# Performance work log

Measured on AMD Instinct MI355X. Metric: run time of the kernel, lower is better.

## Reference

```python
import jax, jax.numpy as jnp
import numpy as np

HEAD_DIM = 128
NUM_HEADS = 16
NUM_KV_HEADS = 8
HIDDEN = 2048
SEQ = 4096
BATCH = 1
ROPE_THETA = 1e6
RMS_EPS = 1e-6


def rms_norm(x, w, eps=RMS_EPS):
    # normalize over the last (head_dim) axis
    var = jnp.mean(jnp.square(x), axis=-1, keepdims=True)
    return x * jax.lax.rsqrt(var + eps) * w


def apply_rope(x, positions):
    # x: [B, S, H, D], positions: [B, S]; rotate-half (GPT-NeoX style)
    d = x.shape[-1]
    inv_freq = 1.0 / (ROPE_THETA ** (jnp.arange(0, d, 2, dtype=jnp.float32) / d))  # [D/2]
    ang = positions.astype(jnp.float32)[..., None] * inv_freq  # [B, S, D/2]
    cos = jnp.cos(ang)[:, :, None, :]  # [B, S, 1, D/2]
    sin = jnp.sin(ang)[:, :, None, :]
    x1, x2 = x[..., : d // 2], x[..., d // 2 :]
    return jnp.concatenate([x1 * cos - x2 * sin, x2 * cos + x1 * sin], axis=-1)


def setup_inputs() -> dict:
    key = jax.random.key(0)
    ks = jax.random.split(key, 8)
    s = 0.02
    return {
        "positions": jnp.broadcast_to(jnp.arange(SEQ, dtype=jnp.int64 if jax.config.jax_enable_x64 else jnp.int32)[None, :], (BATCH, SEQ)),
        "hidden_states": jax.random.normal(ks[0], (BATCH, SEQ, HIDDEN), jnp.float32),
        "wq": jax.random.normal(ks[1], (NUM_HEADS * HEAD_DIM, HIDDEN), jnp.float32) * s,
        "bq": jnp.zeros((NUM_HEADS * HEAD_DIM,), jnp.float32),
        "wk": jax.random.normal(ks[2], (NUM_KV_HEADS * HEAD_DIM, HIDDEN), jnp.float32) * s,
        "bk": jnp.zeros((NUM_KV_HEADS * HEAD_DIM,), jnp.float32),
        "wv": jax.random.normal(ks[3], (NUM_KV_HEADS * HEAD_DIM, HIDDEN), jnp.float32) * s,
        "bv": jnp.zeros((NUM_KV_HEADS * HEAD_DIM,), jnp.float32),
        "wo": jax.random.normal(ks[4], (HIDDEN, NUM_HEADS * HEAD_DIM), jnp.float32) * s,
        "bo": jnp.zeros((HIDDEN,), jnp.float32),
        "q_norm_w": jnp.ones((HEAD_DIM,), jnp.float32),
        "k_norm_w": jnp.ones((HEAD_DIM,), jnp.float32),
    }


def reference(positions, hidden_states, wq, bq, wk, bk, wv, bv, wo, bo, q_norm_w, k_norm_w):
    B, S, _ = hidden_states.shape
    H, Hkv, D = NUM_HEADS, NUM_KV_HEADS, HEAD_DIM
    scaling = D ** -0.5

    q = (hidden_states @ wq.T + bq).reshape(B, S, H, D)
    k = (hidden_states @ wk.T + bk).reshape(B, S, Hkv, D)
    v = (hidden_states @ wv.T + bv).reshape(B, S, Hkv, D)

    q = apply_rope(rms_norm(q, q_norm_w), positions)
    k = apply_rope(rms_norm(k, k_norm_w), positions)

    # GQA: repeat_interleave kv heads to match query heads
    rep = H // Hkv
    k = jnp.repeat(k, rep, axis=2)  # [B, S, H, D]
    v = jnp.repeat(v, rep, axis=2)

    # scores: [B, H, S, S]
    scores = jnp.einsum("bqhd,bkhd->bhqk", q, k) * scaling
    causal = jnp.tril(jnp.ones((S, S), dtype=bool))
    scores = jnp.where(causal[None, None], scores, -jnp.inf)
    attn = jax.nn.softmax(scores, axis=-1)

    out = jnp.einsum("bhqk,bkhd->bqhd", attn, v).reshape(B, S, H * D)
    return out @ wo.T + bo
```

## Files before the change

kernel.cpp:

```cpp
#include <hip/hip_runtime.h>
#include <hip/hip_bf16.h>

#define SQ   4096
#define HIDN 2048
#define NH   16
#define NKV  8
#define HD   128
#define QD   2048
#define KD   1024
#define KVB  64

typedef __bf16 bf16x8 __attribute__((ext_vector_type(8)));
typedef float  f32x4  __attribute__((ext_vector_type(4)));

__device__ __forceinline__ float b2f(unsigned short u) {
    union { float f; unsigned int i; } v; v.i = ((unsigned int)u) << 16; return v.f;
}
__device__ __forceinline__ unsigned short f2b(float f) {
    union { float f; unsigned int i; } v; v.f = f;
    unsigned int i = v.i;
    return (unsigned short)((i + 0x7FFFu + ((i >> 16) & 1u)) >> 16);
}

__device__ __forceinline__ void gload_lds16(const void* g, void* l) {
    __builtin_amdgcn_global_load_lds(
        (const __attribute__((address_space(1))) unsigned int*)g,
        (__attribute__((address_space(3))) unsigned int*)l, 16, 0, 0);
}

#define MFMA16(a, b, c) __builtin_amdgcn_mfma_f32_16x16x32_bf16(a, b, c, 0, 0, 0)

#define DPP_ROR(x, n) __int_as_float(__builtin_amdgcn_update_dpp(            \
    __float_as_int(x), __float_as_int(x), 0x120 + (n), 0xF, 0xF, false))

__device__ __forceinline__ float rowmax16(float x) {
    x = fmaxf(x, DPP_ROR(x, 1));
    x = fmaxf(x, DPP_ROR(x, 2));
    x = fmaxf(x, DPP_ROR(x, 4));
    x = fmaxf(x, DPP_ROR(x, 8));
    return x;
}
__device__ __forceinline__ float rowsum16(float x) {
    x += DPP_ROR(x, 1);
    x += DPP_ROR(x, 2);
    x += DPP_ROR(x, 4);
    x += DPP_ROR(x, 8);
    return x;
}

__global__ __launch_bounds__(256) void cvt_all(const float* __restrict__ h,
                                               const float* __restrict__ wq,
                                               const float* __restrict__ wk,
                                               const float* __restrict__ wv,
                                               const float* __restrict__ wo,
                                               unsigned short* __restrict__ oh,
                                               unsigned short* __restrict__ owq,
                                               unsigned short* __restrict__ owk,
                                               unsigned short* __restrict__ owv,
                                               unsigned short* __restrict__ owo) {
    int i = blockIdx.x * 256 + threadIdx.x;
    const float* src; unsigned short* dst; int off;
    if (i < 2097152)      { src = h;  dst = oh;  off = i; }
    else if (i < 3145728) { src = wq; dst = owq; off = i - 2097152; }
    else if (i < 3670016) { src = wk; dst = owk; off = i - 3145728; }
    else if (i < 4194304) { src = wv; dst = owv; off = i - 3670016; }
    else                  { src = wo; dst = owo; off = i - 4194304; }
    float4 v = ((const float4*)src)[off];
    ushort4 u;
    u.x = f2b(v.x); u.y = f2b(v.y); u.z = f2b(v.z); u.w = f2b(v.w);
    ((ushort4*)dst)[off] = u;
}

__global__ __launch_bounds__(256) void rope_table(const int* __restrict__ pos,
                                                  float* __restrict__ cosT,
                                                  float* __restrict__ sinT) {
    int i = blockIdx.x * 256 + threadIdx.x;
    int s = i >> 6, j = i & 63;
    double invf = exp(-(double)j * (log(1.0e6) / 64.0));
    float a = (float)((double)pos[s] * invf);
    cosT[i] = cosf(a);
    sinT[i] = sinf(a);
}

template <int EPI>
__global__ __launch_bounds__(256) void gemm128(const unsigned short* __restrict__ A,
                                               const unsigned short* __restrict__ B,
                                               const float* __restrict__ bias,
                                               void* __restrict__ Cout,
                                               int M, int N, int K) {
    __shared__ unsigned short As[128 * 32];
    __shared__ unsigned short Bs[128 * 32];
    const int tid = threadIdx.x, wid = tid >> 6, lane = tid & 63;
    const int g = lane >> 4, c = lane & 15;
    const int wr = wid >> 1, wc = wid & 1;
    const int orig = blockIdx.y * gridDim.x + blockIdx.x;
    const int cpx = (gridDim.x * gridDim.y) >> 3;
    const int wg = (orig & 7) * cpx + (orig >> 3);
    const int bx = wg % gridDim.x, by = wg / gridDim.x;
    const long rowbase = (long)by * 128;
    const long colbase = (long)bx * 128;

    f32x4 acc[4][4];
#pragma unroll
    for (int m = 0; m < 4; ++m)
#pragma unroll
        for (int n = 0; n < 4; ++n) acc[m][n] = (f32x4){0.f, 0.f, 0.f, 0.f};

    const int ch0 = (wid * 2) * 64 + lane;
    const int ch1 = (wid * 2 + 1) * 64 + lane;

    for (int kt = 0; kt < K; kt += 32) {
        gload_lds16(A + ((rowbase + (ch0 >> 2)) * K + kt + (ch0 & 3) * 8),
                    As + (wid * 2) * 64 * 8);
        gload_lds16(B + ((colbase + (ch0 >> 2)) * K + kt + (ch0 & 3) * 8),
                    Bs + (wid * 2) * 64 * 8);
        gload_lds16(A + ((rowbase + (ch1 >> 2)) * K + kt + (ch1 & 3) * 8),
                    As + (wid * 2 + 1) * 64 * 8);
        gload_lds16(B + ((colbase + (ch1 >> 2)) * K + kt + (ch1 & 3) * 8),
                    Bs + (wid * 2 + 1) * 64 * 8);
        __syncthreads();
        bf16x8 a[4], b[4];
#pragma unroll
        for (int m = 0; m < 4; ++m)
            a[m] = *(const bf16x8*)(As + (wr * 64 + m * 16 + c) * 32 + g * 8);
#pragma unroll
        for (int n = 0; n < 4; ++n)
            b[n] = *(const bf16x8*)(Bs + (wc * 64 + n * 16 + c) * 32 + g * 8);
#pragma unroll
        for (int m = 0; m < 4; ++m)
#pragma unroll
            for (int n = 0; n < 4; ++n) acc[m][n] = MFMA16(a[m], b[n], acc[m][n]);
        __syncthreads();
    }

#pragma unroll
    for (int m = 0; m < 4; ++m) {
        const long grow0 = rowbase + wr * 64 + m * 16 + g * 4;
#pragma unroll
        for (int n = 0; n < 4; ++n) {
            const long gcol = colbase + wc * 64 + n * 16 + c;
            const float bs = bias[gcol];
            if (EPI == 0) {
                unsigned short* C = (unsigned short*)Cout;
#pragma unroll
                for (int r = 0; r < 4; ++r)
                    C[(grow0 + r) * N + gcol] = f2b(acc[m][n][r] + bs);
            } else if (EPI == 1) {
                float* C = (float*)Cout;
#pragma unroll
                for (int r = 0; r < 4; ++r)
                    C[(grow0 + r) * N + gcol] = acc[m][n][r] + bs;
            } else {
                unsigned short* C = (unsigned short*)Cout;
                ushort4 pk;
                pk.x = f2b(acc[m][n][0] + bs);
                pk.y = f2b(acc[m][n][1] + bs);
                pk.z = f2b(acc[m][n][2] + bs);
                pk.w = f2b(acc[m][n][3] + bs);
                *(ushort4*)(C + gcol * (long)M + grow0) = pk;
            }
        }
    }
}

__global__ __launch_bounds__(256) void norm_rope(const unsigned short* __restrict__ proj,
                                                 int nh,
                                                 const float* __restrict__ w,
                                                 const float* __restrict__ cosT,
                                                 const float* __restrict__ sinT,
                                                 unsigned short* __restrict__ outt,
                                                 float oscale) {
    int wv = (blockIdx.x * 256 + threadIdx.x) >> 6;
    int lane = threadIdx.x & 63;
    int s = wv / nh, h = wv - s * nh;
    const unsigned short* p = proj + (size_t)s * (nh * HD) + h * HD;
    float x1 = b2f(p[lane]);
    float x2 = b2f(p[lane + 64]);
    float ss = x1 * x1 + x2 * x2;
#pragma unroll
    for (int d = 1; d < 64; d <<= 1) ss += __shfl_xor(ss, d);
    float r = rsqrtf(ss * (1.f / 128.f) + 1e-6f);
    x1 *= r * w[lane];
    x2 *= r * w[lane + 64];
    float cs = cosT[s * 64 + lane], sn = sinT[s * 64 + lane];
    unsigned short o1 = f2b((x1 * cs - x2 * sn) * oscale);
    unsigned short o2 = f2b((x2 * cs + x1 * sn) * oscale);
    unsigned short* q = outt + ((size_t)h * SQ + s) * HD;
    q[lane] = o1;
    q[lane + 64] = o2;
}

__global__ __launch_bounds__(256, 2) void fattn(const unsigned short* __restrict__ qt,
                                                const unsigned short* __restrict__ kt,
                                                const unsigned short* __restrict__ vt,
                                                unsigned short* __restrict__ aout) {
    __shared__ unsigned short Ks[2][KVB * HD];
    __shared__ unsigned short Vs[2][HD * KVB];
    __shared__ unsigned short Pl[4][32][64];
    const int tid = threadIdx.x, wid = tid >> 6, lane = tid & 63;
    const int g = lane >> 4, c = lane & 15;
    const int id = blockIdx.x;
    const int qb = (id < 256) ? (id >> 4) : (31 - ((id - 256) >> 4));
    const int h = id & 15, hk = h >> 1;
    const int qrow0 = qb * 128 + wid * 32;
    const unsigned short* qh = qt + (size_t)h * SQ * HD;
    const unsigned short* kh = kt + (size_t)hk * SQ * HD;
    const unsigned short* vh = vt + (size_t)hk * HD * SQ;
    const int ntile = 2 * qb + 2;
    char* plw = (char*)&Pl[wid][0][0];

    bf16x8 qa[2][4];
#pragma unroll
    for (int m = 0; m < 2; ++m)
#pragma unroll
        for (int ks = 0; ks < 4; ++ks)
            qa[m][ks] = *(const bf16x8*)(qh + (size_t)(qrow0 + m * 16 + c) * HD + ks * 32 + g * 8);

    f32x4 o[2][8];
#pragma unroll
    for (int m = 0; m < 2; ++m)
#pragma unroll
        for (int df = 0; df < 8; ++df) o[m][df] = (f32x4){0.f, 0.f, 0.f, 0.f};
    float mrow[2][4], lrow[2][4];
#pragma unroll
    for (int m = 0; m < 2; ++m)
#pragma unroll
        for (int r = 0; r < 4; ++r) { mrow[m][r] = -1e30f; lrow[m][r] = 0.f; }

    auto stage = [&](int b, int t) {
        const int kv0 = t * KVB;
#pragma unroll
        for (int i = 0; i < 4; ++i) {
            const int gi = wid * 4 + i;
            const int P = gi * 1024 + lane * 16;
            const int rk = P >> 8;
            const int Uk = (P & 255) ^ (((rk >> 2) & 7) << 4);
            gload_lds16(kh + (size_t)(kv0 + rk) * HD + (Uk >> 1),
                        (char*)Ks[b] + gi * 1024);
            const int rv = P >> 7;
            const int Uv = (P & 127) ^ ((rv & 7) << 4);
            gload_lds16(vh + (size_t)rv * SQ + kv0 + (Uv >> 1),
                        (char*)Vs[b] + gi * 1024);
        }
    };

    stage(0, 0);
    asm volatile("s_waitcnt vmcnt(0)" ::: "memory");
    __syncthreads();

    int bcur = 0;
    for (int j = 0; j < ntile; ++j) {
        const int kv0 = j * KVB;
        if (j + 1 < ntile) stage(bcur ^ 1, j + 1);

        if (kv0 <= qrow0 + 31) {
            f32x4 sa[2][4];
#pragma unroll
            for (int m = 0; m < 2; ++m)
#pragma unroll
                for (int nf = 0; nf < 4; ++nf) sa[m][nf] = (f32x4){0.f, 0.f, 0.f, 0.f};
            __builtin_amdgcn_s_setprio(1);
#pragma unroll
            for (int nf = 0; nf < 4; ++nf) {
                const int row = (c << 2) + nf;
                const int key = (c & 7) << 4;
#pragma unroll
                for (int ks = 0; ks < 4; ++ks) {
                    bf16x8 kf = *(const bf16x8*)((const char*)Ks[bcur] + row * 256 +
                                                 ((ks * 64 + g * 16) ^ key));
                    sa[0][nf] = MFMA16(qa[0][ks], kf, sa[0][nf]);
                    sa[1][nf] = MFMA16(qa[1][ks], kf, sa[1][nf]);
                }
            }
            __builtin_amdgcn_s_setprio(0);
            if (kv0 + 63 > qrow0) {
#pragma unroll
                for (int m = 0; m < 2; ++m)
#pragma unroll
                    for (int nf = 0; nf < 4; ++nf) {
                        const int col = kv0 + (c << 2) + nf;
#pragma unroll
                        for (int r = 0; r < 4; ++r) {
                            int row = qrow0 + m * 16 + g * 4 + r;
                            if (col > row) sa[m][nf][r] = -1e30f;
                        }
                    }
            }
            float nmax[2][4];
            int small = 1;
#pragma unroll
            for (int m = 0; m < 2; ++m)
#pragma unroll
                for (int r = 0; r < 4; ++r) {
                    float mx = fmaxf(fmaxf(sa[m][0][r], sa[m][1][r]),
                                     fmaxf(sa[m][2][r], sa[m][3][r]));
                    mx = rowmax16(mx);
                    nmax[m][r] = mx;
                    small &= (mx <= mrow[m][r] + 8.0f);
                }
            if (!__all(small)) {
                float psc[2][4];
#pragma unroll
                for (int m = 0; m < 2; ++m)
#pragma unroll
                    for (int r = 0; r < 4; ++r) {
                        float mn = fmaxf(mrow[m][r], nmax[m][r]);
                        psc[m][r] = __builtin_amdgcn_exp2f(mrow[m][r] - mn);
                        mrow[m][r] = mn;
                        lrow[m][r] *= psc[m][r];
                    }
#pragma unroll
                for (int m = 0; m < 2; ++m)
#pragma unroll
                    for (int df = 0; df < 8; ++df)
#pragma unroll
                        for (int r = 0; r < 4; ++r) o[m][df][r] *= psc[m][r];
            }
#pragma unroll
            for (int m = 0; m < 2; ++m)
#pragma unroll
                for (int r = 0; r < 4; ++r) {
                    float rs = 0.f;
#pragma unroll
                    for (int nf = 0; nf < 4; ++nf) {
                        float p = __builtin_amdgcn_exp2f(sa[m][nf][r] - mrow[m][r]);
                        sa[m][nf][r] = p;
                        rs += p;
                    }
                    lrow[m][r] += rowsum16(rs);
                }
#pragma unroll
            for (int m = 0; m < 2; ++m)
#pragma unroll
                for (int r = 0; r < 4; ++r) {
                    unsigned int lo, hi;
                    asm("v_cvt_pk_bf16_f32 %0, %1, %2"
                        : "=v"(lo) : "v"(sa[m][0][r]), "v"(sa[m][1][r]));
                    asm("v_cvt_pk_bf16_f32 %0, %1, %2"
                        : "=v"(hi) : "v"(sa[m][2][r]), "v"(sa[m][3][r]));
                    const int row = m * 16 + g * 4 + r;
                    const int pcol = (c * 8) ^ ((row & 7) << 4);
                    *(uint2*)(plw + row * 128 + pcol) = make_uint2(lo, hi);
                }
            __builtin_amdgcn_s_setprio(1);
#pragma unroll
            for (int ks = 0; ks < 2; ++ks) {
                bf16x8 pa0 = *(const bf16x8*)(plw + (0 * 16 + c) * 128 +
                                              ((ks * 64 + g * 16) ^ ((c & 7) << 4)));
                bf16x8 pa1 = *(const bf16x8*)(plw + (1 * 16 + c) * 128 +
                                              ((ks * 64 + g * 16) ^ ((c & 7) << 4)));
#pragma unroll
                for (int df = 0; df < 8; ++df) {
                    const int rd = df * 16 + c;
                    bf16x8 vb = *(const bf16x8*)((const char*)Vs[bcur] + rd * 128 +
                                                 ((ks * 64 + g * 16) ^ ((rd & 7) << 4)));
                    o[0][df] = MFMA16(pa0, vb, o[0][df]);
                    o[1][df] = MFMA16(pa1, vb, o[1][df]);
                }
            }
            __builtin_amdgcn_s_setprio(0);
        }
        asm volatile("s_waitcnt vmcnt(0)" ::: "memory");
        __syncthreads();
        bcur ^= 1;
    }

    float inv[2][4];
#pragma unroll
    for (int m = 0; m < 2; ++m)
#pragma unroll
        for (int r = 0; r < 4; ++r) inv[m][r] = 1.f / lrow[m][r];
#pragma unroll
    for (int m = 0; m < 2; ++m)
#pragma unroll
        for (int df = 0; df < 8; ++df)
#pragma unroll
            for (int r = 0; r < 4; ++r) {
                size_t row = qrow0 + m * 16 + g * 4 + r;
                aout[row * QD + h * HD + df * 16 + c] = f2b(o[m][df][r] * inv[m][r]);
            }
}

extern "C" void kernel_launch(void* const* d_in, const int* in_sizes, int n_in,
                              void* d_out, int out_size, void* d_ws, size_t ws_size,
                              hipStream_t stream) {
    const int*   positions = (const int*)d_in[0];
    const float* hidden    = (const float*)d_in[1];
    const float* wq        = (const float*)d_in[2];
    const float* bq        = (const float*)d_in[3];
    const float* wk        = (const float*)d_in[4];
    const float* bk        = (const float*)d_in[5];
    const float* wv        = (const float*)d_in[6];
    const float* bv        = (const float*)d_in[7];
    const float* wo        = (const float*)d_in[8];
    const float* bo        = (const float*)d_in[9];
    const float* qnw       = (const float*)d_in[10];
    const float* knw       = (const float*)d_in[11];
    float* out = (float*)d_out;

    char* w = (char*)d_ws;
    unsigned short* hidden_b = (unsigned short*)(w);
    unsigned short* wq_b     = (unsigned short*)(w + 16777216);
    unsigned short* wk_b     = (unsigned short*)(w + 25165824);
    unsigned short* wv_b     = (unsigned short*)(w + 29360128);
    unsigned short* wo_b     = (unsigned short*)(w + 33554432);
    unsigned short* qproj    = (unsigned short*)(w + 41943040);
    unsigned short* kproj    = (unsigned short*)(w + 58720256);
    unsigned short* q_t      = (unsigned short*)(w + 67108864);
    unsigned short* k_t      = (unsigned short*)(w + 83886080);
    unsigned short* v_t      = (unsigned short*)(w + 92274688);
    float*          cosT     = (float*)(w + 100663296);
    float*          sinT     = (float*)(w + 101711872);
    unsigned short* attn     = qproj;

    cvt_all<<<20480, 256, 0, stream>>>(hidden, wq, wk, wv, wo,
                                       hidden_b, wq_b, wk_b, wv_b, wo_b);
    rope_table<<<SQ * 64 / 256, 256, 0, stream>>>(positions, cosT, sinT);
    gemm128<0><<<dim3(QD / 128, SQ / 128), 256, 0, stream>>>(hidden_b, wq_b, bq, qproj, SQ, QD, HIDN);
    gemm128<0><<<dim3(KD / 128, SQ / 128), 256, 0, stream>>>(hidden_b, wk_b, bk, kproj, SQ, KD, HIDN);
    gemm128<2><<<dim3(KD / 128, SQ / 128), 256, 0, stream>>>(hidden_b, wv_b, bv, v_t, SQ, KD, HIDN);
    norm_rope<<<SQ * NH / 4, 256, 0, stream>>>(qproj, NH, qnw, cosT, sinT, q_t,
                                               (float)(0.08838834764831845 * 1.4426950408889634));
    norm_rope<<<SQ * NKV / 4, 256, 0, stream>>>(kproj, NKV, knw, cosT, sinT, k_t, 1.0f);
    fattn<<<512, 256, 0, stream>>>(q_t, k_t, v_t, attn);
    gemm128<1><<<dim3(QD / 128, SQ / 128), 256, 0, stream>>>(attn, wo_b, bo, out, SQ, QD, HIDN);
}
```

Measured before the change: 517.2 us.

## Fuse QKV GEMMs, reuse K LDS for P, reorder attention blocks, float rope table

After: 474.5 us. -8.3%, faster.

```diff
diff --git a/kernel.cpp b/kernel.cpp
--- a/kernel.cpp
+++ b/kernel.cpp
@@ -76,18 +76,21 @@
                                                   float* __restrict__ sinT) {
     int i = blockIdx.x * 256 + threadIdx.x;
     int s = i >> 6, j = i & 63;
-    double invf = exp(-(double)j * (log(1.0e6) / 64.0));
-    float a = (float)((double)pos[s] * invf);
+    float invf = __expf(-(float)j * (1.3815510557964274f / 6.4f));
+    float a = (float)pos[s] * invf;
     cosT[i] = cosf(a);
     sinT[i] = sinf(a);
 }
 
-template <int EPI>
-__global__ __launch_bounds__(256) void gemm128(const unsigned short* __restrict__ A,
-                                               const unsigned short* __restrict__ B,
-                                               const float* __restrict__ bias,
-                                               void* __restrict__ Cout,
-                                               int M, int N, int K) {
+__global__ __launch_bounds__(256) void gemm_qkv(const unsigned short* __restrict__ A,
+                                                const unsigned short* __restrict__ B,
+                                                const float* __restrict__ bq,
+                                                const float* __restrict__ bk,
+                                                const float* __restrict__ bv,
+                                                unsigned short* __restrict__ qp,
+                                                unsigned short* __restrict__ kp,
+                                                unsigned short* __restrict__ vtp) {
+    const int M = 4096, K = 2048;
     __shared__ unsigned short As[128 * 32];
     __shared__ unsigned short Bs[128 * 32];
     const int tid = threadIdx.x, wid = tid >> 6, lane = tid & 63;
@@ -139,26 +142,89 @@
 #pragma unroll
         for (int n = 0; n < 4; ++n) {
             const long gcol = colbase + wc * 64 + n * 16 + c;
-            const float bs = bias[gcol];
-            if (EPI == 0) {
-                unsigned short* C = (unsigned short*)Cout;
+            if (colbase < 2048) {
+                const float bs = bq[gcol];
 #pragma unroll
                 for (int r = 0; r < 4; ++r)
-                    C[(grow0 + r) * N + gcol] = f2b(acc[m][n][r] + bs);
-            } else if (EPI == 1) {
-                float* C = (float*)Cout;
+                    qp[(grow0 + r) * QD + gcol] = f2b(acc[m][n][r] + bs);
+            } else if (colbase < 3072) {
+                const float bs = bk[gcol - 2048];
 #pragma unroll
                 for (int r = 0; r < 4; ++r)
-                    C[(grow0 + r) * N + gcol] = acc[m][n][r] + bs;
+                    kp[(grow0 + r) * KD + (gcol - 2048)] = f2b(acc[m][n][r] + bs);
             } else {
-                unsigned short* C = (unsigned short*)Cout;
+                const float bs = bv[gcol - 3072];
                 ushort4 pk;
                 pk.x = f2b(acc[m][n][0] + bs);
                 pk.y = f2b(acc[m][n][1] + bs);
                 pk.z = f2b(acc[m][n][2] + bs);
                 pk.w = f2b(acc[m][n][3] + bs);
-                *(ushort4*)(C + gcol * (long)M + grow0) = pk;
-            }
+                *(ushort4*)(vtp + (gcol - 3072) * (long)M + grow0) = pk;
+            }
+        }
+    }
+}
+
+__global__ __launch_bounds__(256) void gemm_o(const unsigned short* __restrict__ A,
+                                              const unsigned short* __restrict__ B,
+                                              const float* __restrict__ bias,
+                                              float* __restrict__ Cout,
+                                              int M, int N, int K) {
+    __shared__ unsigned short As[128 * 32];
+    __shared__ unsigned short Bs[128 * 32];
+    const int tid = threadIdx.x, wid = tid >> 6, lane = tid & 63;
+    const int g = lane >> 4, c = lane & 15;
+    const int wr = wid >> 1, wc = wid & 1;
+    const int orig = blockIdx.y * gridDim.x + blockIdx.x;
+    const int cpx = (gridDim.x * gridDim.y) >> 3;
+    const int wg = (orig & 7) * cpx + (orig >> 3);
+    const int bx = wg % gridDim.x, by = wg / gridDim.x;
+    const long rowbase = (long)by * 128;
+    const long colbase = (long)bx * 128;
+
+    f32x4 acc[4][4];
+#pragma unroll
+    for (int m = 0; m < 4; ++m)
+#pragma unroll
+        for (int n = 0; n < 4; ++n) acc[m][n] = (f32x4){0.f, 0.f, 0.f, 0.f};
+
+    const int ch0 = (wid * 2) * 64 + lane;
+    const int ch1 = (wid * 2 + 1) * 64 + lane;
+
+    for (int kt = 0; kt < K; kt += 32) {
+        gload_lds16(A + ((rowbase + (ch0 >> 2)) * K + kt + (ch0 & 3) * 8),
+                    As + (wid * 2) * 64 * 8);
+        gload_lds16(B + ((colbase + (ch0 >> 2)) * K + kt + (ch0 & 3) * 8),
+                    Bs + (wid * 2) * 64 * 8);
+        gload_lds16(A + ((rowbase + (ch1 >> 2)) * K + kt + (ch1 & 3) * 8),
+                    As + (wid * 2 + 1) * 64 * 8);
+        gload_lds16(B + ((colbase + (ch1 >> 2)) * K + kt + (ch1 & 3) * 8),
+                    Bs + (wid * 2 + 1) * 64 * 8);
+        __syncthreads();
+        bf16x8 a[4], b[4];
+#pragma unroll
+        for (int m = 0; m < 4; ++m)
+            a[m] = *(const bf16x8*)(As + (wr * 64 + m * 16 + c) * 32 + g * 8);
+#pragma unroll
+        for (int n = 0; n < 4; ++n)
+            b[n] = *(const bf16x8*)(Bs + (wc * 64 + n * 16 + c) * 32 + g * 8);
+#pragma unroll
+        for (int m = 0; m < 4; ++m)
+#pragma unroll
+            for (int n = 0; n < 4; ++n) acc[m][n] = MFMA16(a[m], b[n], acc[m][n]);
+        __syncthreads();
+    }
+
+#pragma unroll
+    for (int m = 0; m < 4; ++m) {
+        const long grow0 = rowbase + wr * 64 + m * 16 + g * 4;
+#pragma unroll
+        for (int n = 0; n < 4; ++n) {
+            const long gcol = colbase + wc * 64 + n * 16 + c;
+            const float bs = bias[gcol];
+#pragma unroll
+            for (int r = 0; r < 4; ++r)
+                Cout[(grow0 + r) * N + gcol] = acc[m][n][r] + bs;
         }
     }
 }
@@ -196,25 +262,23 @@
                                                 unsigned short* __restrict__ aout) {
     __shared__ unsigned short Ks[2][KVB * HD];
     __shared__ unsigned short Vs[2][HD * KVB];
-    __shared__ unsigned short Pl[4][32][64];
     const int tid = threadIdx.x, wid = tid >> 6, lane = tid & 63;
     const int g = lane >> 4, c = lane & 15;
     const int id = blockIdx.x;
-    const int qb = (id < 256) ? (id >> 4) : (31 - ((id - 256) >> 4));
+    const int qb = (id < 256) ? (31 - (id >> 4)) : ((id - 256) >> 4);
     const int h = id & 15, hk = h >> 1;
-    const int qrow0 = qb * 128 + wid * 32;
+    const int row0 = qb * 128 + wid * 32;
     const unsigned short* qh = qt + (size_t)h * SQ * HD;
     const unsigned short* kh = kt + (size_t)hk * SQ * HD;
     const unsigned short* vh = vt + (size_t)hk * HD * SQ;
     const int ntile = 2 * qb + 2;
-    char* plw = (char*)&Pl[wid][0][0];
 
     bf16x8 qa[2][4];
 #pragma unroll
-    for (int m = 0; m < 2; ++m)
-#pragma unroll
-        for (int ks = 0; ks < 4; ++ks)
-            qa[m][ks] = *(const bf16x8*)(qh + (size_t)(qrow0 + m * 16 + c) * HD + ks * 32 + g * 8);
+    for (int ks = 0; ks < 4; ++ks) {
+        qa[0][ks] = *(const bf16x8*)(qh + (size_t)(row0 + c) * HD + ks * 32 + g * 8);
+        qa[1][ks] = *(const bf16x8*)(qh + (size_t)(row0 + 16 + c) * HD + ks * 32 + g * 8);
+    }
 
     f32x4 o[2][8];
 #pragma unroll
@@ -253,132 +317,136 @@
         const int kv0 = j * KVB;
         if (j + 1 < ntile) stage(bcur ^ 1, j + 1);
 
-        if (kv0 <= qrow0 + 31) {
-            f32x4 sa[2][4];
-#pragma unroll
-            for (int m = 0; m < 2; ++m)
-#pragma unroll
-                for (int nf = 0; nf < 4; ++nf) sa[m][nf] = (f32x4){0.f, 0.f, 0.f, 0.f};
-            __builtin_amdgcn_s_setprio(1);
-#pragma unroll
-            for (int nf = 0; nf < 4; ++nf) {
-                const int row = (c << 2) + nf;
-                const int key = (c & 7) << 4;
-#pragma unroll
-                for (int ks = 0; ks < 4; ++ks) {
-                    bf16x8 kf = *(const bf16x8*)((const char*)Ks[bcur] + row * 256 +
-                                                 ((ks * 64 + g * 16) ^ key));
-                    sa[0][nf] = MFMA16(qa[0][ks], kf, sa[0][nf]);
-                    sa[1][nf] = MFMA16(qa[1][ks], kf, sa[1][nf]);
+        f32x4 sa[2][4];
+#pragma unroll
+        for (int m = 0; m < 2; ++m)
+#pragma unroll
+            for (int nf = 0; nf < 4; ++nf) sa[m][nf] = (f32x4){0.f, 0.f, 0.f, 0.f};
+        __builtin_amdgcn_s_setprio(1);
+#pragma unroll
+        for (int nf = 0; nf < 4; ++nf) {
+            const int krow = (c << 2) + nf;
+            const int key = (c & 7) << 4;
+#pragma unroll
+            for (int ks = 0; ks < 4; ++ks) {
+                bf16x8 kf = *(const bf16x8*)((const char*)Ks[bcur] + krow * 256 +
+                                             ((ks * 64 + g * 16) ^ key));
+                sa[0][nf] = MFMA16(qa[0][ks], kf, sa[0][nf]);
+                sa[1][nf] = MFMA16(qa[1][ks], kf, sa[1][nf]);
+            }
+        }
+        __builtin_amdgcn_s_setprio(0);
+        asm volatile("s_waitcnt lgkmcnt(0)" ::: "memory");
+        __builtin_amdgcn_s_barrier();
+        char* plw = (char*)Ks[bcur] + wid * 4096;
+
+        if (kv0 + 63 > row0) {
+#pragma unroll
+            for (int m = 0; m < 2; ++m) {
+                const int rb = row0 + m * 16;
+#pragma unroll
+                for (int nf = 0; nf < 4; ++nf) {
+                    const int col = kv0 + (c << 2) + nf;
+#pragma unroll
+                    for (int r = 0; r < 4; ++r) {
+                        int row = rb + g * 4 + r;
+                        if (col > row) sa[m][nf][r] = -1e30f;
+                    }
                 }
             }
-            __builtin_amdgcn_s_setprio(0);
-            if (kv0 + 63 > qrow0) {
-#pragma unroll
-                for (int m = 0; m < 2; ++m)
-#pragma unroll
-                    for (int nf = 0; nf < 4; ++nf) {
-                        const int col = kv0 + (c << 2) + nf;
-#pragma unroll
-                        for (int r = 0; r < 4; ++r) {
-                            int row = qrow0 + m * 16 + g * 4 + r;
-                            if (col > row) sa[m][nf][r] = -1e30f;
-                        }
-                    }
-            }
-            float nmax[2][4];
-            int small = 1;
-#pragma unroll
-            for (int m = 0; m < 2; ++m)
+        }
+        float nmax[2][4];
+        int small = 1;
+#pragma unroll
+        for (int m = 0; m < 2; ++m)
+#pragma unroll
+            for (int r = 0; r < 4; ++r) {
+                float mx = fmaxf(fmaxf(sa[m][0][r], sa[m][1][r]),
+                                 fmaxf(sa[m][2][r], sa[m][3][r]));
+                mx = rowmax16(mx);
+                nmax[m][r] = mx;
+                small &= (mx <= mrow[m][r] + 8.0f);
+            }
+        if (!__all(small)) {
+#pragma unroll
+            for (int m = 0; m < 2; ++m) {
+                float psc[4];
 #pragma unroll
                 for (int r = 0; r < 4; ++r) {
-                    float mx = fmaxf(fmaxf(sa[m][0][r], sa[m][1][r]),
-                                     fmaxf(sa[m][2][r], sa[m][3][r]));
-                    mx = rowmax16(mx);
-                    nmax[m][r] = mx;
-                    small &= (mx <= mrow[m][r] + 8.0f);
+                    float mn = fmaxf(mrow[m][r], nmax[m][r]);
+                    psc[r] = __builtin_amdgcn_exp2f(mrow[m][r] - mn);
+                    mrow[m][r] = mn;
+                    lrow[m][r] *= psc[r];
                 }
-            if (!__all(small)) {
-                float psc[2][4];
-#pragma unroll
-                for (int m = 0; m < 2; ++m)
-#pragma unroll
-                    for (int r = 0; r < 4; ++r) {
-                        float mn = fmaxf(mrow[m][r], nmax[m][r]);
-                        psc[m][r] = __builtin_amdgcn_exp2f(mrow[m][r] - mn);
-                        mrow[m][r] = mn;
-                        lrow[m][r] *= psc[m][r];
-                    }
-#pragma unroll
-                for (int m = 0; m < 2; ++m)
-#pragma unroll
-                    for (int df = 0; df < 8; ++df)
-#pragma unroll
-                        for (int r = 0; r < 4; ++r) o[m][df][r] *= psc[m][r];
-            }
-#pragma unroll
-            for (int m = 0; m < 2; ++m)
-#pragma unroll
-                for (int r = 0; r < 4; ++r) {
-                    float rs = 0.f;
-#pragma unroll
-                    for (int nf = 0; nf < 4; ++nf) {
-                        float p = __builtin_amdgcn_exp2f(sa[m][nf][r] - mrow[m][r]);
-                        sa[m][nf][r] = p;
-                        rs += p;
-                    }
-                    lrow[m][r] += rowsum16(rs);
+#pragma unroll
+                for (int df = 0; df < 8; ++df)
+#pragma unroll
+                    for (int r = 0; r < 4; ++r) o[m][df][r] *= psc[r];
+            }
+        }
+#pragma unroll
+        for (int m = 0; m < 2; ++m)
+#pragma unroll
+            for (int r = 0; r < 4; ++r) {
+                float rs = 0.f;
+#pragma unroll
+                for (int nf = 0; nf < 4; ++nf) {
+                    float p = __builtin_amdgcn_exp2f(sa[m][nf][r] - mrow[m][r]);
+                    sa[m][nf][r] = p;
+                    rs += p;
                 }
-#pragma unroll
-            for (int m = 0; m < 2; ++m)
-#pragma unroll
-                for (int r = 0; r < 4; ++r) {
-                    unsigned int lo, hi;
-                    asm("v_cvt_pk_bf16_f32 %0, %1, %2"
-                        : "=v"(lo) : "v"(sa[m][0][r]), "v"(sa[m][1][r]));
-                    asm("v_cvt_pk_bf16_f32 %0, %1, %2"
-                        : "=v"(hi) : "v"(sa[m][2][r]), "v"(sa[m][3][r]));
-                    const int row = m * 16 + g * 4 + r;
-                    const int pcol = (c * 8) ^ ((row & 7) << 4);
-                    *(uint2*)(plw + row * 128 + pcol) = make_uint2(lo, hi);
-                }
-            __builtin_amdgcn_s_setprio(1);
-#pragma unroll
-            for (int ks = 0; ks < 2; ++ks) {
-                bf16x8 pa0 = *(const bf16x8*)(plw + (0 * 16 + c) * 128 +
-                                              ((ks * 64 + g * 16) ^ ((c & 7) << 4)));
-                bf16x8 pa1 = *(const bf16x8*)(plw + (1 * 16 + c) * 128 +
-                                              ((ks * 64 + g * 16) ^ ((c & 7) << 4)));
-#pragma unroll
-                for (int df = 0; df < 8; ++df) {
-                    const int rd = df * 16 + c;
-                    bf16x8 vb = *(const bf16x8*)((const char*)Vs[bcur] + rd * 128 +
-                                                 ((ks * 64 + g * 16) ^ ((rd & 7) << 4)));
-                    o[0][df] = MFMA16(pa0, vb, o[0][df]);
-                    o[1][df] = MFMA16(pa1, vb, o[1][df]);
-                }
-            }
-            __builtin_amdgcn_s_setprio(0);
-        }
+                lrow[m][r] += rowsum16(rs);
+            }
+#pragma unroll
+        for (int m = 0; m < 2; ++m)
+#pragma unroll
+            for (int r = 0; r < 4; ++r) {
+                unsigned int lo, hi;
+                asm("v_cvt_pk_bf16_f32 %0, %1, %2"
+                    : "=v"(lo) : "v"(sa[m][0][r]), "v"(sa[m][1][r]));
+                asm("v_cvt_pk_bf16_f32 %0, %1, %2"
+                    : "=v"(hi) : "v"(sa[m][2][r]), "v"(sa[m][3][r]));
+                const int row = m * 16 + g * 4 + r;
+                const int pcol = (c * 8) ^ ((row & 7) << 4);
+                *(uint2*)(plw + row * 128 + pcol) = make_uint2(lo, hi);
+            }
+        asm volatile("s_waitcnt lgkmcnt(0)" ::: "memory");
+        __builtin_amdgcn_s_setprio(1);
+#pragma unroll
+        for (int ks = 0; ks < 2; ++ks) {
+            const int pk_ = (ks * 64 + g * 16) ^ ((c & 7) << 4);
+            bf16x8 pa0 = *(const bf16x8*)(plw + c * 128 + pk_);
+            bf16x8 pa1 = *(const bf16x8*)(plw + (16 + c) * 128 + pk_);
+#pragma unroll
+            for (int df = 0; df < 8; ++df) {
+                const int rd = df * 16 + c;
+                bf16x8 vb = *(const bf16x8*)((const char*)Vs[bcur] + rd * 128 +
+                                             ((ks * 64 + g * 16) ^ ((rd & 7) << 4)));
+                o[0][df] = MFMA16(pa0, vb, o[0][df]);
+                o[1][df] = MFMA16(pa1, vb, o[1][df]);
+            }
+        }
+        __builtin_amdgcn_s_setprio(0);
+
         asm volatile("s_waitcnt vmcnt(0)" ::: "memory");
         __syncthreads();
         bcur ^= 1;
     }
 
-    float inv[2][4];
-#pragma unroll
-    for (int m = 0; m < 2; ++m)
-#pragma unroll
-        for (int r = 0; r < 4; ++r) inv[m][r] = 1.f / lrow[m][r];
-#pragma unroll
-    for (int m = 0; m < 2; ++m)
+#pragma unroll
+    for (int m = 0; m < 2; ++m) {
+        const int rb = row0 + m * 16;
+        float inv[4];
+#pragma unroll
+        for (int r = 0; r < 4; ++r) inv[r] = 1.f / lrow[m][r];
 #pragma unroll
         for (int df = 0; df < 8; ++df)
 #pragma unroll
             for (int r = 0; r < 4; ++r) {
-                size_t row = qrow0 + m * 16 + g * 4 + r;
-                aout[row * QD + h * HD + df * 16 + c] = f2b(o[m][df][r] * inv[m][r]);
-            }
+                size_t row = rb + g * 4 + r;
+                aout[row * QD + h * HD + df * 16 + c] = f2b(o[m][df][r] * inv[r]);
+            }
+    }
 }
 
 extern "C" void kernel_launch(void* const* d_in, const int* in_sizes, int n_in,
@@ -400,6 +468,7 @@
 
     char* w = (char*)d_ws;
     unsigned short* hidden_b = (unsigned short*)(w);
+    unsigned short* wqkv_b   = (unsigned short*)(w + 16777216);
     unsigned short* wq_b     = (unsigned short*)(w + 16777216);
     unsigned short* wk_b     = (unsigned short*)(w + 25165824);
     unsigned short* wv_b     = (unsigned short*)(w + 29360128);
@@ -416,12 +485,11 @@
     cvt_all<<<20480, 256, 0, stream>>>(hidden, wq, wk, wv, wo,
                                        hidden_b, wq_b, wk_b, wv_b, wo_b);
     rope_table<<<SQ * 64 / 256, 256, 0, stream>>>(positions, cosT, sinT);
-    gemm128<0><<<dim3(QD / 128, SQ / 128), 256, 0, stream>>>(hidden_b, wq_b, bq, qproj, SQ, QD, HIDN);
-    gemm128<0><<<dim3(KD / 128, SQ / 128), 256, 0, stream>>>(hidden_b, wk_b, bk, kproj, SQ, KD, HIDN);
-    gemm128<2><<<dim3(KD / 128, SQ / 128), 256, 0, stream>>>(hidden_b, wv_b, bv, v_t, SQ, KD, HIDN);
+    gemm_qkv<<<dim3(32, 32), 256, 0, stream>>>(hidden_b, wqkv_b, bq, bk, bv,
+                                               qproj, kproj, v_t);
     norm_rope<<<SQ * NH / 4, 256, 0, stream>>>(qproj, NH, qnw, cosT, sinT, q_t,
                                                (float)(0.08838834764831845 * 1.4426950408889634));
     norm_rope<<<SQ * NKV / 4, 256, 0, stream>>>(kproj, NKV, knw, cosT, sinT, k_t, 1.0f);
     fattn<<<512, 256, 0, stream>>>(q_t, k_t, v_t, attn);
-    gemm128<1><<<dim3(QD / 128, SQ / 128), 256, 0, stream>>>(attn, wo_b, bo, out, SQ, QD, HIDN);
-}
+    gemm_o<<<dim3(QD / 128, SQ / 128), 256, 0, stream>>>(attn, wo_b, bo, out, SQ, QD, HIDN);
+}
```
